# Kernel tuning notes

Hardware: AMD Instinct MI355X
Metric: run time of the kernel (lower is better)

## Reference

```python
import jax, jax.numpy as jnp
import numpy as np

CODEBOOK_SIZE = 256
EMBED_DIM = 32
N_TOKENS = 524288
EPS = 1e-6


def l2norm(t, eps=EPS):
    # F.normalize(p=2): x / max(||x||, eps)
    n = jnp.sqrt(jnp.sum(t * t, axis=-1, keepdims=True))
    return t / jnp.maximum(n, eps)


def setup_inputs() -> dict:
    key = jax.random.key(0)
    kx, kw = jax.random.split(key)
    x = jax.random.normal(kx, (N_TOKENS, EMBED_DIM), dtype=jnp.float32)
    # embedding.weight.data.uniform_(-1/codebook_size, 1/codebook_size)
    codebook = jax.random.uniform(
        kw, (CODEBOOK_SIZE, EMBED_DIM), dtype=jnp.float32,
        minval=-1.0 / CODEBOOK_SIZE, maxval=1.0 / CODEBOOK_SIZE)
    return {"x": x, "codebook": codebook}


def reference(x, codebook):
    # --- find_nearest_codes: cdist + argmin + gather ---
    # squared euclidean distances have the same argmin as torch.cdist
    x2 = jnp.sum(x * x, axis=-1, keepdims=True)            # [N, 1]
    c2 = jnp.sum(codebook * codebook, axis=-1)             # [K]
    d2 = x2 - 2.0 * (x @ codebook.T) + c2[None, :]         # [N, K]
    indices = jnp.argmin(d2, axis=1)                       # [N] int
    quantized = codebook[indices]                          # [N, D]

    # --- update_usage: histogram over codes ---
    counts = jnp.zeros((CODEBOOK_SIZE,), dtype=jnp.float32).at[indices].add(1.0)

    # --- rotate_to(x, quantized): rotation-trick gradient estimator ---
    u = jax.lax.stop_gradient(l2norm(x))                   # detached direction of src
    q = jax.lax.stop_gradient(l2norm(quantized))           # detached direction of tgt
    w = jax.lax.stop_gradient(l2norm(u + q))               # Householder bisector, detached
    e = x                                                  # gradient flows through e only
    ew = jnp.sum(e * w, axis=-1, keepdims=True)            # (e @ w_col)
    eu = jnp.sum(e * u, axis=-1, keepdims=True)            # (e @ u_col)
    rotated = e - 2.0 * ew * w + 2.0 * eu * q              # [N, D]

    return rotated, indices, counts
```

## Files before the change

### kernel.cpp

```cpp
#include <hip/hip_runtime.h>

#define N_TOK   524288
#define KC      256
#define D       32
#define EPSF    1e-6f
#define TPT     64
#define NTILES  (N_TOK / TPT)
#define NBLK    768
#define BLKT    256

__global__ __launch_bounds__(BLKT) void vq_main(
    const float* __restrict__ x, const float* __restrict__ cb,
    float* __restrict__ out_rot, float* __restrict__ out_idx,
    float* __restrict__ ws_hist, float* __restrict__ out_cnt, int use_ws)
{
    __shared__ float ct[D][KC];
    __shared__ float c2s[KC];
    __shared__ float xt[2][D][TPT];
    __shared__ float x2s[2][TPT];
    __shared__ float hist[KC];

    const int tid  = threadIdx.x;
    const int lane = tid & 63;

    {
#pragma clang fp contract(off)
        const float4* cb4 = (const float4*)(cb + (size_t)tid * D);
        float4 r[8];
#pragma unroll
        for (int j = 0; j < 8; j++) r[j] = cb4[j];
        float t[32];
#pragma unroll
        for (int j = 0; j < 8; j++) {
            t[4 * j + 0] = r[j].x * r[j].x;
            t[4 * j + 1] = r[j].y * r[j].y;
            t[4 * j + 2] = r[j].z * r[j].z;
            t[4 * j + 3] = r[j].w * r[j].w;
        }
        float pr[8];
#pragma unroll
        for (int j = 0; j < 8; j++)
            pr[j] = ((t[j] + t[j + 8]) + t[j + 16]) + t[j + 24];
        c2s[tid] = ((pr[0] + pr[1]) + (pr[2] + pr[3])) + ((pr[4] + pr[5]) + (pr[6] + pr[7]));
#pragma unroll
        for (int j = 0; j < 8; j++) {
            ct[4 * j + 0][tid] = r[j].x;
            ct[4 * j + 1][tid] = r[j].y;
            ct[4 * j + 2][tid] = r[j].z;
            ct[4 * j + 3][tid] = r[j].w;
        }
        hist[tid] = 0.f;
    }

    const int tt   = tid >> 4;
    const int tc   = tid & 15;
    const int tok  = tid >> 2;
    const int sub  = tid & 3;
    const int colw = tok ^ (sub << 4);

    auto stage = [&](int buf, float4 a, float4 b) {
#pragma clang fp contract(off)
        float xs[8] = {a.x, a.y, a.z, a.w, b.x, b.y, b.z, b.w};
        const int k0 = sub * 8;
#pragma unroll
        for (int j = 0; j < 8; j++) xt[buf][k0 + j][colw] = xs[j];
        float sq[8];
#pragma unroll
        for (int j = 0; j < 8; j++) sq[j] = xs[j] * xs[j];
        const int base = lane & ~3;
        float pr[8];
#pragma unroll
        for (int j = 0; j < 8; j++) {
            float t01 = sq[j] + __shfl_xor(sq[j], 1, 64);
            float s2  = __shfl(sq[j], base + 2, 64);
            float s3  = __shfl(sq[j], base + 3, 64);
            pr[j] = (t01 + s2) + s3;
        }
        float v = ((pr[0] + pr[1]) + (pr[2] + pr[3])) + ((pr[4] + pr[5]) + (pr[6] + pr[7]));
        if (sub == 0) x2s[buf][tok] = v;
    };

    float4 aC, bC;
    {
        const float4* xg = (const float4*)(x + (size_t)blockIdx.x * TPT * D + (size_t)tid * 8);
        aC = xg[0]; bC = xg[1];
    }
    stage(0, aC, bC);
    __syncthreads();

    int cur = 0;
    for (int tile = blockIdx.x; tile < NTILES; tile += gridDim.x) {
        const int nt = tile + gridDim.x;
        const bool hasN = (nt < NTILES);
        float4 aN = aC, bN = bC;
        if (hasN) {
            const float4* xg = (const float4*)(x + (size_t)nt * TPT * D + (size_t)tid * 8);
            aN = xg[0]; bN = xg[1];
        }

        float x4[4];
#pragma unroll
        for (int i = 0; i < 4; i++) x4[i] = x2s[cur][tt * 4 + i];

        float acc[4][16];
#pragma unroll
        for (int i = 0; i < 4; i++)
#pragma unroll
            for (int j = 0; j < 16; j++) acc[i][j] = 0.f;

#pragma unroll 4
        for (int k = 0; k < D; k++) {
            const int xcol = (tt * 4) ^ ((k >> 3) << 4);
            const float4 xv = *(const float4*)&xt[cur][k][xcol];
            const float4 v0 = *(const float4*)&ct[k][tc * 4];
            const float4 v1 = *(const float4*)&ct[k][64 + tc * 4];
            const float4 v2 = *(const float4*)&ct[k][128 + tc * 4];
            const float4 v3 = *(const float4*)&ct[k][192 + tc * 4];
            const float xs[4]  = {xv.x, xv.y, xv.z, xv.w};
            const float cs[16] = {v0.x, v0.y, v0.z, v0.w, v1.x, v1.y, v1.z, v1.w,
                                  v2.x, v2.y, v2.z, v2.w, v3.x, v3.y, v3.z, v3.w};
#pragma unroll
            for (int i = 0; i < 4; i++)
#pragma unroll
                for (int j = 0; j < 16; j++)
                    acc[i][j] = __builtin_fmaf(xs[i], cs[j], acc[i][j]);
        }

        float bestv[4] = {3.4e38f, 3.4e38f, 3.4e38f, 3.4e38f};
        int   besti[4] = {0x7fffffff, 0x7fffffff, 0x7fffffff, 0x7fffffff};
#pragma unroll
        for (int j = 0; j < 16; j++) {
            const int code = (j >> 2) * 64 + tc * 4 + (j & 3);
            const float c2v = c2s[code];
#pragma unroll
            for (int i = 0; i < 4; i++) {
                float t2 = x4[i] - 2.0f * acc[i][j];
                float s  = t2 + c2v;
                if (s < bestv[i]) { bestv[i] = s; besti[i] = code; }
            }
        }

#pragma unroll
        for (int m = 1; m < 16; m <<= 1) {
#pragma unroll
            for (int i = 0; i < 4; i++) {
                float ov = __shfl_xor(bestv[i], m, 64);
                int   oi = __shfl_xor(besti[i], m, 64);
                if (ov < bestv[i] || (ov == bestv[i] && oi < besti[i])) {
                    bestv[i] = ov; besti[i] = oi;
                }
            }
        }

        const int src = lane & 48;
        const int b0 = __shfl(besti[0], src, 64);
        const int b1 = __shfl(besti[1], src, 64);
        const int b2 = __shfl(besti[2], src, 64);
        const int b3 = __shfl(besti[3], src, 64);
        const int ii = (lane >> 2) & 3;
        const int bi = (ii == 0) ? b0 : (ii == 1) ? b1 : (ii == 2) ? b2 : b3;

        {
            const size_t gtok = (size_t)tile * TPT + tok;
            const float4* cg = (const float4*)(cb + (size_t)bi * D + sub * 8);
            float4 ca = cg[0], cbv = cg[1];

            float xs8[8] = {aC.x, aC.y, aC.z, aC.w, bC.x, bC.y, bC.z, bC.w};
            float cs8[8] = {ca.x, ca.y, ca.z, ca.w, cbv.x, cbv.y, cbv.z, cbv.w};

            float px2 = 0.f, pc2 = 0.f;
#pragma unroll
            for (int j = 0; j < 8; j++) { px2 = fmaf(xs8[j], xs8[j], px2); pc2 = fmaf(cs8[j], cs8[j], pc2); }
            float x2 = px2 + __shfl_xor(px2, 1, 64); x2 += __shfl_xor(x2, 2, 64);
            float c2 = pc2 + __shfl_xor(pc2, 1, 64); c2 += __shfl_xor(c2, 2, 64);
            const float inx = 1.f / fmaxf(sqrtf(x2), EPSF);
            const float inc = 1.f / fmaxf(sqrtf(c2), EPSF);

            float us8[8], qs8[8], ws8[8];
            float pw2 = 0.f;
#pragma unroll
            for (int j = 0; j < 8; j++) {
                us8[j] = xs8[j] * inx;
                qs8[j] = cs8[j] * inc;
                ws8[j] = us8[j] + qs8[j];
                pw2 = fmaf(ws8[j], ws8[j], pw2);
            }
            float w2 = pw2 + __shfl_xor(pw2, 1, 64); w2 += __shfl_xor(w2, 2, 64);
            const float inw = 1.f / fmaxf(sqrtf(w2), EPSF);

            float pew = 0.f, peu = 0.f;
#pragma unroll
            for (int j = 0; j < 8; j++) {
                ws8[j] *= inw;
                pew = fmaf(xs8[j], ws8[j], pew);
                peu = fmaf(xs8[j], us8[j], peu);
            }
            float ew = pew + __shfl_xor(pew, 1, 64); ew += __shfl_xor(ew, 2, 64);
            float eu = peu + __shfl_xor(peu, 1, 64); eu += __shfl_xor(eu, 2, 64);

            float ro[8];
#pragma unroll
            for (int j = 0; j < 8; j++)
                ro[j] = xs8[j] - 2.f * ew * ws8[j] + 2.f * eu * qs8[j];

            float4* og = (float4*)(out_rot + gtok * D + sub * 8);
            og[0] = make_float4(ro[0], ro[1], ro[2], ro[3]);
            og[1] = make_float4(ro[4], ro[5], ro[6], ro[7]);

            if (sub == 0) {
                out_idx[gtok] = (float)bi;
                atomicAdd(&hist[bi], 1.f);
            }
        }

        if (hasN) stage(cur ^ 1, aN, bN);
        __syncthreads();
        aC = aN; bC = bN; cur ^= 1;
    }

    if (use_ws) ws_hist[(size_t)blockIdx.x * KC + tid] = hist[tid];
    else        atomicAdd(&out_cnt[tid], hist[tid]);
}

__global__ __launch_bounds__(256) void vq_reduce(const float* __restrict__ ws,
                                                 float* __restrict__ out_cnt)
{
    const int c = blockIdx.x * 8 + (threadIdx.x >> 5);
    const int l = threadIdx.x & 31;
    float s = 0.f;
    for (int b = l; b < NBLK; b += 32) s += ws[(size_t)b * KC + c];
#pragma unroll
    for (int m = 1; m < 32; m <<= 1) s += __shfl_xor(s, m, 64);
    if (l == 0) out_cnt[c] = s;
}

extern "C" void kernel_launch(void* const* d_in, const int* in_sizes, int n_in,
                              void* d_out, int out_size, void* d_ws, size_t ws_size,
                              hipStream_t stream)
{
    const float* x  = (const float*)d_in[0];
    const float* cb = (const float*)d_in[1];
    float* out      = (float*)d_out;
    float* out_rot  = out;
    float* out_idx  = out + (size_t)N_TOK * D;
    float* out_cnt  = out_idx + N_TOK;

    const size_t ws_need = (size_t)NBLK * KC * sizeof(float);
    const int use_ws = (ws_size >= ws_need) ? 1 : 0;
    if (!use_ws) hipMemsetAsync(out_cnt, 0, KC * sizeof(float), stream);

    vq_main<<<NBLK, BLKT, 0, stream>>>(x, cb, out_rot, out_idx,
                                       (float*)d_ws, out_cnt, use_ws);
    if (use_ws) vq_reduce<<<32, 256, 0, stream>>>((const float*)d_ws, out_cnt);
}
```

Before: 244.8 us.

## Double token tile to 128 with an 8x16 register microtile per thread

Doubles the tokens per tile from 64 to 128. Each thread now accumulates 8 tokens by 16 codes, so the codebook values read from LDS are reused twice as much per load. The per-token epilogue moves from 4 threads to 2 threads per token, which halves its shuffle reductions, and the best index is now picked by a register select tree instead of cross-lane shuffles. In exchange, register pressure goes up (128 accumulators, launch bounds set to 2 blocks), the grid shrinks to 512 blocks, and the XOR swizzle on the staged x tile is dropped, which may add LDS bank conflicts.

```diff
diff --git a/kernel.cpp b/kernel.cpp
--- a/kernel.cpp
+++ b/kernel.cpp
@@ -4,12 +4,12 @@
 #define KC      256
 #define D       32
 #define EPSF    1e-6f
-#define TPT     64
+#define TPT     128
 #define NTILES  (N_TOK / TPT)
-#define NBLK    768
+#define NBLK    512
 #define BLKT    256
 
-__global__ __launch_bounds__(BLKT) void vq_main(
+__global__ __launch_bounds__(BLKT, 2) void vq_main(
     const float* __restrict__ x, const float* __restrict__ cb,
     float* __restrict__ out_rot, float* __restrict__ out_idx,
     float* __restrict__ ws_hist, float* __restrict__ out_cnt, int use_ws)
@@ -21,7 +21,6 @@
     __shared__ float hist[KC];
 
     const int tid  = threadIdx.x;
-    const int lane = tid & 63;
 
     {
 #pragma clang fp contract(off)
@@ -52,88 +51,89 @@
         hist[tid] = 0.f;
     }
 
-    const int tt   = tid >> 4;
-    const int tc   = tid & 15;
-    const int tok  = tid >> 2;
-    const int sub  = tid & 3;
-    const int colw = tok ^ (sub << 4);
-
-    auto stage = [&](int buf, float4 a, float4 b) {
+    const int tt  = tid >> 4;
+    const int tc  = tid & 15;
+    const int tok = tid >> 1;
+    const int sub = tid & 1;
+    const int k0  = sub * 16;
+
+    auto stage = [&](int buf, float4 r0, float4 r1, float4 r2, float4 r3) {
 #pragma clang fp contract(off)
-        float xs[8] = {a.x, a.y, a.z, a.w, b.x, b.y, b.z, b.w};
-        const int k0 = sub * 8;
-#pragma unroll
-        for (int j = 0; j < 8; j++) xt[buf][k0 + j][colw] = xs[j];
-        float sq[8];
-#pragma unroll
-        for (int j = 0; j < 8; j++) sq[j] = xs[j] * xs[j];
-        const int base = lane & ~3;
+        float xs[16] = {r0.x, r0.y, r0.z, r0.w, r1.x, r1.y, r1.z, r1.w,
+                        r2.x, r2.y, r2.z, r2.w, r3.x, r3.y, r3.z, r3.w};
+#pragma unroll
+        for (int j = 0; j < 16; j++) xt[buf][k0 + j][tok] = xs[j];
+        float sq[16];
+#pragma unroll
+        for (int j = 0; j < 16; j++) sq[j] = xs[j] * xs[j];
         float pr[8];
 #pragma unroll
         for (int j = 0; j < 8; j++) {
-            float t01 = sq[j] + __shfl_xor(sq[j], 1, 64);
-            float s2  = __shfl(sq[j], base + 2, 64);
-            float s3  = __shfl(sq[j], base + 3, 64);
-            pr[j] = (t01 + s2) + s3;
-        }
-        float v = ((pr[0] + pr[1]) + (pr[2] + pr[3])) + ((pr[4] + pr[5]) + (pr[6] + pr[7]));
-        if (sub == 0) x2s[buf][tok] = v;
+            float a = sq[j] + sq[j + 8];
+            float u = __shfl_xor(sq[j], 1, 64);
+            float v = __shfl_xor(sq[j + 8], 1, 64);
+            pr[j] = (a + u) + v;
+        }
+        float x2v = ((pr[0] + pr[1]) + (pr[2] + pr[3])) + ((pr[4] + pr[5]) + (pr[6] + pr[7]));
+        if (sub == 0) x2s[buf][tok] = x2v;
     };
 
-    float4 aC, bC;
+    float4 aC0, aC1, aC2, aC3;
     {
-        const float4* xg = (const float4*)(x + (size_t)blockIdx.x * TPT * D + (size_t)tid * 8);
-        aC = xg[0]; bC = xg[1];
+        const float4* xg = (const float4*)(x + (size_t)blockIdx.x * TPT * D + (size_t)tid * 16);
+        aC0 = xg[0]; aC1 = xg[1]; aC2 = xg[2]; aC3 = xg[3];
     }
-    stage(0, aC, bC);
+    stage(0, aC0, aC1, aC2, aC3);
     __syncthreads();
 
     int cur = 0;
     for (int tile = blockIdx.x; tile < NTILES; tile += gridDim.x) {
         const int nt = tile + gridDim.x;
         const bool hasN = (nt < NTILES);
-        float4 aN = aC, bN = bC;
+        float4 aN0 = aC0, aN1 = aC1, aN2 = aC2, aN3 = aC3;
         if (hasN) {
-            const float4* xg = (const float4*)(x + (size_t)nt * TPT * D + (size_t)tid * 8);
-            aN = xg[0]; bN = xg[1];
-        }
-
-        float x4[4];
-#pragma unroll
-        for (int i = 0; i < 4; i++) x4[i] = x2s[cur][tt * 4 + i];
-
-        float acc[4][16];
-#pragma unroll
-        for (int i = 0; i < 4; i++)
+            const float4* xg = (const float4*)(x + (size_t)nt * TPT * D + (size_t)tid * 16);
+            aN0 = xg[0]; aN1 = xg[1]; aN2 = xg[2]; aN3 = xg[3];
+        }
+
+        float x4[8];
+#pragma unroll
+        for (int i = 0; i < 8; i++) x4[i] = x2s[cur][tt * 8 + i];
+
+        float acc[8][16];
+#pragma unroll
+        for (int i = 0; i < 8; i++)
 #pragma unroll
             for (int j = 0; j < 16; j++) acc[i][j] = 0.f;
 
 #pragma unroll 4
         for (int k = 0; k < D; k++) {
-            const int xcol = (tt * 4) ^ ((k >> 3) << 4);
-            const float4 xv = *(const float4*)&xt[cur][k][xcol];
+            const float4 xv0 = *(const float4*)&xt[cur][k][tt * 8];
+            const float4 xv1 = *(const float4*)&xt[cur][k][tt * 8 + 4];
             const float4 v0 = *(const float4*)&ct[k][tc * 4];
             const float4 v1 = *(const float4*)&ct[k][64 + tc * 4];
             const float4 v2 = *(const float4*)&ct[k][128 + tc * 4];
             const float4 v3 = *(const float4*)&ct[k][192 + tc * 4];
-            const float xs[4]  = {xv.x, xv.y, xv.z, xv.w};
+            const float xs[8]  = {xv0.x, xv0.y, xv0.z, xv0.w, xv1.x, xv1.y, xv1.z, xv1.w};
             const float cs[16] = {v0.x, v0.y, v0.z, v0.w, v1.x, v1.y, v1.z, v1.w,
                                   v2.x, v2.y, v2.z, v2.w, v3.x, v3.y, v3.z, v3.w};
 #pragma unroll
-            for (int i = 0; i < 4; i++)
+            for (int i = 0; i < 8; i++)
 #pragma unroll
                 for (int j = 0; j < 16; j++)
                     acc[i][j] = __builtin_fmaf(xs[i], cs[j], acc[i][j]);
         }
 
-        float bestv[4] = {3.4e38f, 3.4e38f, 3.4e38f, 3.4e38f};
-        int   besti[4] = {0x7fffffff, 0x7fffffff, 0x7fffffff, 0x7fffffff};
+        float bestv[8];
+        int   besti[8];
+#pragma unroll
+        for (int i = 0; i < 8; i++) { bestv[i] = 3.4e38f; besti[i] = 0x7fffffff; }
 #pragma unroll
         for (int j = 0; j < 16; j++) {
             const int code = (j >> 2) * 64 + tc * 4 + (j & 3);
             const float c2v = c2s[code];
 #pragma unroll
-            for (int i = 0; i < 4; i++) {
+            for (int i = 0; i < 8; i++) {
                 float t2 = x4[i] - 2.0f * acc[i][j];
                 float s  = t2 + c2v;
                 if (s < bestv[i]) { bestv[i] = s; besti[i] = code; }
@@ -143,7 +143,7 @@
 #pragma unroll
         for (int m = 1; m < 16; m <<= 1) {
 #pragma unroll
-            for (int i = 0; i < 4; i++) {
+            for (int i = 0; i < 8; i++) {
                 float ov = __shfl_xor(bestv[i], m, 64);
                 int   oi = __shfl_xor(besti[i], m, 64);
                 if (ov < bestv[i] || (ov == bestv[i] && oi < besti[i])) {
@@ -152,60 +152,70 @@
             }
         }
 
-        const int src = lane & 48;
-        const int b0 = __shfl(besti[0], src, 64);
-        const int b1 = __shfl(besti[1], src, 64);
-        const int b2 = __shfl(besti[2], src, 64);
-        const int b3 = __shfl(besti[3], src, 64);
-        const int ii = (lane >> 2) & 3;
-        const int bi = (ii == 0) ? b0 : (ii == 1) ? b1 : (ii == 2) ? b2 : b3;
+        const bool b0 = (tid >> 1) & 1;
+        const bool b1 = (tid >> 2) & 1;
+        const bool b2 = (tid >> 3) & 1;
+        const int s0  = b0 ? besti[1] : besti[0];
+        const int s1  = b0 ? besti[3] : besti[2];
+        const int s2  = b0 ? besti[5] : besti[4];
+        const int s3  = b0 ? besti[7] : besti[6];
+        const int s01 = b1 ? s1 : s0;
+        const int s23 = b1 ? s3 : s2;
+        const int bi  = b2 ? s23 : s01;
 
         {
             const size_t gtok = (size_t)tile * TPT + tok;
-            const float4* cg = (const float4*)(cb + (size_t)bi * D + sub * 8);
-            float4 ca = cg[0], cbv = cg[1];
-
-            float xs8[8] = {aC.x, aC.y, aC.z, aC.w, bC.x, bC.y, bC.z, bC.w};
-            float cs8[8] = {ca.x, ca.y, ca.z, ca.w, cbv.x, cbv.y, cbv.z, cbv.w};
+            const float4* cg = (const float4*)(cb + (size_t)bi * D + k0);
+            float4 c0 = cg[0], c1 = cg[1], c2f = cg[2], c3 = cg[3];
+
+            float xs16[16] = {aC0.x, aC0.y, aC0.z, aC0.w, aC1.x, aC1.y, aC1.z, aC1.w,
+                              aC2.x, aC2.y, aC2.z, aC2.w, aC3.x, aC3.y, aC3.z, aC3.w};
+            float cs16[16] = {c0.x, c0.y, c0.z, c0.w, c1.x, c1.y, c1.z, c1.w,
+                              c2f.x, c2f.y, c2f.z, c2f.w, c3.x, c3.y, c3.z, c3.w};
 
             float px2 = 0.f, pc2 = 0.f;
 #pragma unroll
-            for (int j = 0; j < 8; j++) { px2 = fmaf(xs8[j], xs8[j], px2); pc2 = fmaf(cs8[j], cs8[j], pc2); }
-            float x2 = px2 + __shfl_xor(px2, 1, 64); x2 += __shfl_xor(x2, 2, 64);
-            float c2 = pc2 + __shfl_xor(pc2, 1, 64); c2 += __shfl_xor(c2, 2, 64);
+            for (int j = 0; j < 16; j++) {
+                px2 = fmaf(xs16[j], xs16[j], px2);
+                pc2 = fmaf(cs16[j], cs16[j], pc2);
+            }
+            float x2 = px2 + __shfl_xor(px2, 1, 64);
+            float c2 = pc2 + __shfl_xor(pc2, 1, 64);
             const float inx = 1.f / fmaxf(sqrtf(x2), EPSF);
             const float inc = 1.f / fmaxf(sqrtf(c2), EPSF);
 
-            float us8[8], qs8[8], ws8[8];
+            float us16[16], qs16[16], ws16[16];
             float pw2 = 0.f;
 #pragma unroll
-            for (int j = 0; j < 8; j++) {
-                us8[j] = xs8[j] * inx;
-                qs8[j] = cs8[j] * inc;
-                ws8[j] = us8[j] + qs8[j];
-                pw2 = fmaf(ws8[j], ws8[j], pw2);
-            }
-            float w2 = pw2 + __shfl_xor(pw2, 1, 64); w2 += __shfl_xor(w2, 2, 64);
+            for (int j = 0; j < 16; j++) {
+                us16[j] = xs16[j] * inx;
+                qs16[j] = cs16[j] * inc;
+                ws16[j] = us16[j] + qs16[j];
+                pw2 = fmaf(ws16[j], ws16[j], pw2);
+            }
+            float w2 = pw2 + __shfl_xor(pw2, 1, 64);
             const float inw = 1.f / fmaxf(sqrtf(w2), EPSF);
 
             float pew = 0.f, peu = 0.f;
 #pragma unroll
-            for (int j = 0; j < 8; j++) {
-                ws8[j] *= inw;
-                pew = fmaf(xs8[j], ws8[j], pew);
-                peu = fmaf(xs8[j], us8[j], peu);
-            }
-            float ew = pew + __shfl_xor(pew, 1, 64); ew += __shfl_xor(ew, 2, 64);
-            float eu = peu + __shfl_xor(peu, 1, 64); eu += __shfl_xor(eu, 2, 64);
-
-            float ro[8];
-#pragma unroll
-            for (int j = 0; j < 8; j++)
-                ro[j] = xs8[j] - 2.f * ew * ws8[j] + 2.f * eu * qs8[j];
-
-            float4* og = (float4*)(out_rot + gtok * D + sub * 8);
-            og[0] = make_float4(ro[0], ro[1], ro[2], ro[3]);
-            og[1] = make_float4(ro[4], ro[5], ro[6], ro[7]);
+            for (int j = 0; j < 16; j++) {
+                ws16[j] *= inw;
+                pew = fmaf(xs16[j], ws16[j], pew);
+                peu = fmaf(xs16[j], us16[j], peu);
+            }
+            float ew = pew + __shfl_xor(pew, 1, 64);
+            float eu = peu + __shfl_xor(peu, 1, 64);
+
+            float ro[16];
+#pragma unroll
+            for (int j = 0; j < 16; j++)
+                ro[j] = xs16[j] - 2.f * ew * ws16[j] + 2.f * eu * qs16[j];
+
+            float4* og = (float4*)(out_rot + gtok * D + k0);
+            og[0] = make_float4(ro[0],  ro[1],  ro[2],  ro[3]);
+            og[1] = make_float4(ro[4],  ro[5],  ro[6],  ro[7]);
+            og[2] = make_float4(ro[8],  ro[9],  ro[10], ro[11]);
+            og[3] = make_float4(ro[12], ro[13], ro[14], ro[15]);
 
             if (sub == 0) {
                 out_idx[gtok] = (float)bi;
@@ -213,9 +223,10 @@
             }
         }
 
-        if (hasN) stage(cur ^ 1, aN, bN);
+        if (hasN) stage(cur ^ 1, aN0, aN1, aN2, aN3);
         __syncthreads();
-        aC = aN; bC = bN; cur ^= 1;
+        aC0 = aN0; aC1 = aN1; aC2 = aN2; aC3 = aN3;
+        cur ^= 1;
     }
 
     if (use_ws) ws_hist[(size_t)blockIdx.x * KC + tid] = hist[tid];
```

Result: slower. 251.4 us (+2.7%).
